# Kernel optimization log

Measured on AMD Instinct MI355X. Metric: run time of the kernel, lower is better.

Reference implementation:

```python
import jax, jax.numpy as jnp
import numpy as np

DT = 0.05      # bsde.delta_t
EPS = 1e-6     # BatchNormalization epsilon


def _bn(x, gamma, beta):
    # training-mode batch norm: statistics over the batch axis
    m = jnp.mean(x, axis=0, keepdims=True)
    v = jnp.var(x, axis=0, keepdims=True)
    return (x - m) * jax.lax.rsqrt(v + EPS) * gamma + beta


def _subnet(x, g0, b0, W0, g1, b1, W1, g2, b2, W2, bias2, g3, b3):
    # bn -> (dense -> bn -> relu) x 2 -> dense(+bias) -> bn
    x = _bn(x, g0, b0)
    x = jax.nn.relu(_bn(x @ W0, g1, b1))
    x = jax.nn.relu(_bn(x @ W1, g2, b2))
    x = _bn(x @ W2 + bias2, g3, b3)
    return x


def setup_inputs() -> dict:
    key = jax.random.key(0)
    B, D, N, H = 8192, 100, 20, 110
    T = N - 1  # number of subnets
    ks = jax.random.split(key, 18)
    u = lambda k, s, lo, hi: jax.random.uniform(k, s, jnp.float32, lo, hi)
    s_dh = np.sqrt(2.0 / (D + H)).astype(np.float32)
    s_hh = np.sqrt(2.0 / (H + H)).astype(np.float32)
    s_hd = np.sqrt(2.0 / (H + D)).astype(np.float32)
    return {
        "dw": jax.random.normal(ks[0], (B, D, N), jnp.float32) * np.sqrt(DT).astype(np.float32),
        "x": jax.random.normal(ks[1], (B, D, N + 1), jnp.float32),
        "mean_y_input": jax.random.normal(ks[2], (N,), jnp.float32),
        "y_init": u(ks[3], (1,), 0.0, 1.0),
        "z_init": u(ks[4], (1, D), -0.1, 0.1),
        "gamma0": u(ks[5], (T, D), 0.1, 0.5),
        "beta0": 0.1 * jax.random.normal(ks[6], (T, D), jnp.float32),
        "W0": s_dh * jax.random.normal(ks[7], (T, D, H), jnp.float32),
        "gamma1": u(ks[8], (T, H), 0.1, 0.5),
        "beta1": 0.1 * jax.random.normal(ks[9], (T, H), jnp.float32),
        "W1": s_hh * jax.random.normal(ks[10], (T, H, H), jnp.float32),
        "gamma2": u(ks[11], (T, H), 0.1, 0.5),
        "beta2": 0.1 * jax.random.normal(ks[12], (T, H), jnp.float32),
        "W2": s_hd * jax.random.normal(ks[13], (T, H, D), jnp.float32),
        "bias2": jnp.zeros((T, D), jnp.float32),
        "gamma3": u(ks[14], (T, D), 0.1, 0.5),
        "beta3": 0.1 * jax.random.normal(ks[15], (T, D), jnp.float32),
    }


def reference(dw, x, mean_y_input, y_init, z_init, gamma0, beta0, W0,
              gamma1, beta1, W1, gamma2, beta2, W2, bias2, gamma3, beta3):
    B, D, N = dw.shape
    T = N - 1
    # z at step t+1 depends only on x[:, :, t+1] and subnet t -> compute all in parallel
    x_steps = jnp.moveaxis(x[:, :, 1:N], 2, 0)  # [T, B, D]
    z_all = jax.vmap(_subnet)(x_steps, gamma0, beta0, W0, gamma1, beta1, W1,
                              gamma2, beta2, W2, bias2, gamma3, beta3) / D  # [T, B, D]
    z0 = jnp.broadcast_to(z_init, (B, D))          # all_one_vec @ z_init
    zs = jnp.concatenate([z0[None], z_all], axis=0)  # [N, B, D] (z used at each update)
    dw_steps = jnp.moveaxis(dw, 2, 0)               # [N, B, D]
    y0 = jnp.ones((B, 1), dw.dtype) * y_init

    def step(y, zd):
        z, dwt = zd
        # f_tf(t, x, y, z) = sin(y) for the SineBM equation
        y_new = y - DT * jnp.sin(y) + jnp.sum(z * dwt, axis=1, keepdims=True)
        return y_new, jnp.mean(y_new)

    y_final, means = jax.lax.scan(step, y0, (zs, dw_steps))
    mean_y = jnp.concatenate([jnp.mean(y0)[None], means[:T]])  # length N
    return y_final, mean_y
```

## Files before the change

### kernel.cpp

```cpp
#include <hip/hip_runtime.h>

typedef unsigned short u16;
typedef unsigned int   u32;

#define BATCH  8192
#define DIM    100
#define HID    110
#define TSUB   19
#define NSTEP  20
#define KP     128
#define NPAD   112
#define BN_EPS 1e-6f
#define DT_C   0.05f

#define SAB  1024
#define SAR  (BATCH / SAB)
#define SLICES 32

#define A3P  101

typedef __bf16 v8bf __attribute__((ext_vector_type(8)));
typedef float  v4f  __attribute__((ext_vector_type(4)));
typedef u16    u16x4 __attribute__((ext_vector_type(4)));

__device__ __forceinline__ u16 f2bf(float f) {
    u32 u = __float_as_uint(f);
    return (u16)((u + 0x7fffu + ((u >> 16) & 1u)) >> 16);
}
__device__ __forceinline__ float bf2f(u16 h) {
    return __uint_as_float(((u32)h) << 16);
}
__device__ __forceinline__ void acc4(float4& s, float4& q, float4 v) {
    s.x += v.x; s.y += v.y; s.z += v.z; s.w += v.w;
    q.x += v.x * v.x; q.y += v.y * v.y; q.z += v.z * v.z; q.w += v.w * v.w;
}

__global__ void statsA(const float* __restrict__ x, float* __restrict__ part,
                       u32* __restrict__ xT32) {
    __shared__ u16 xls[SAR][2112];
    const int tid = threadIdx.x;
    const int b0 = blockIdx.x * SAR;
    float4 s0 = {0,0,0,0}, q0 = {0,0,0,0};
    float4 s1 = {0,0,0,0}, q1 = {0,0,0,0};
    float4 s2 = {0,0,0,0}, q2 = {0,0,0,0};
#pragma unroll
    for (int r = 0; r < SAR; r++) {
        const float4* row = (const float4*)(x + (size_t)(b0 + r) * 2100);
        float4 v0 = row[tid];
        float4 v1 = row[tid + 256];
        acc4(s0, q0, v0);
        acc4(s1, q1, v1);
        u16x4 p0 = { f2bf(v0.x), f2bf(v0.y), f2bf(v0.z), f2bf(v0.w) };
        u16x4 p1 = { f2bf(v1.x), f2bf(v1.y), f2bf(v1.z), f2bf(v1.w) };
        *(u16x4*)&xls[r][tid * 4]        = p0;
        *(u16x4*)&xls[r][1024 + tid * 4] = p1;
        if (tid < 13) {
            float4 v2 = row[tid + 512];
            acc4(s2, q2, v2);
            u16x4 p2 = { f2bf(v2.x), f2bf(v2.y), f2bf(v2.z), f2bf(v2.w) };
            *(u16x4*)&xls[r][2048 + tid * 4] = p2;
        }
    }
    float* ps = part + (size_t)blockIdx.x * 4200;
    *(float4*)&ps[tid * 4]               = s0;
    *(float4*)&ps[1024 + tid * 4]        = s1;
    *(float4*)&ps[2100 + tid * 4]        = q0;
    *(float4*)&ps[2100 + 1024 + tid * 4] = q1;
    if (tid < 13) {
        *(float4*)&ps[2048 + tid * 4]        = s2;
        *(float4*)&ps[2100 + 2048 + tid * 4] = q2;
    }
    __syncthreads();
    const int TOT = TSUB * SAR * (NPAD / 2);
    for (int i = tid; i < TOT; i += 256) {
        int w = i % (NPAD / 2);
        int seg = i / (NPAD / 2);
        int r = seg % SAR, t = seg / SAR;
        int d0 = w * 2;
        u32 v = 0;
        if (d0 < DIM) {
            u16 lo = xls[r][d0 * 21 + t + 1];
            u16 hi = (d0 + 1 < DIM) ? xls[r][(d0 + 1) * 21 + t + 1] : (u16)0;
            v = (u32)lo | ((u32)hi << 16);
        }
        xT32[((size_t)t * BATCH + b0 + r) * (NPAD / 2) + w] = v;
    }
}

__global__ void statsB(const float* __restrict__ part, float* __restrict__ out) {
    int gid = blockIdx.x * 256 + threadIdx.x;
    if (gid >= 4200 * SLICES) return;
    int slice = gid / 4200;
    int o = gid - slice * 4200;
    const float* p = part + (size_t)slice * (SAB / SLICES) * 4200 + o;
    float acc = 0.f;
#pragma unroll 4
    for (int i = 0; i < SAB / SLICES; i++) acc += p[(size_t)i * 4200];
    atomicAdd(&out[o], acc);
}

__global__ void wtrans(const float* __restrict__ W0, const float* __restrict__ W1,
                       const float* __restrict__ W2, u16* __restrict__ WTsw) {
    __shared__ float lw[HID * HID];
    const int t = blockIdx.x, l = blockIdx.y, tid = threadIdx.x;
    const float* W; int K, N;
    if (l == 0)      { W = W0; K = DIM; N = HID; }
    else if (l == 1) { W = W1; K = HID; N = HID; }
    else             { W = W2; K = HID; N = DIM; }
    const float* Wt = W + (size_t)t * K * N;
    for (int i = tid; i < K * N; i += 256) lw[i] = Wt[i];
    __syncthreads();
    u16* out = WTsw + ((size_t)l * TSUB + t) * (NPAD * KP);
    for (int i = tid; i < NPAD * 16; i += 256) {
        int n = i / 16, p = i % 16;
        int kc = p ^ (n & 7);
        u16 o8[8];
#pragma unroll
        for (int j = 0; j < 8; j++) {
            int k = kc * 8 + j;
            float v = (k < K && n < N) ? lw[k * N + n] : 0.f;
            o8[j] = f2bf(v);
        }
        *(uint4*)&out[(size_t)n * KP + p * 8] = *(uint4*)o8;
    }
}

template <int KREAL, int NOUT, int IDXMODE, int RELU>
__global__ void gemm_kernel(const u16* __restrict__ Ain,
                            const u16* __restrict__ WTswL,
                            const float* __restrict__ sumIn,
                            const float* __restrict__ sqIn,
                            const float* __restrict__ gIn,
                            const float* __restrict__ bIn,
                            u16* __restrict__ Hout,
                            float* __restrict__ sumArr,
                            float* __restrict__ sqArr) {
    __shared__ __align__(16) u16 Alds[128 * KP];
    __shared__ __align__(16) u16 Blds[NPAD * KP];
    __shared__ float s_sum[NPAD], s_sq[NPAD];
    __shared__ float aAffL[KP], cAffL[KP];

    const int tid = threadIdx.x;
    const int mt = blockIdx.x;
    const int t  = blockIdx.y;
    const int brow0 = mt * 128;

    if (tid < NPAD) { s_sum[tid] = 0.f; s_sq[tid] = 0.f; }
    if (tid < KREAL) {
        int idx = (IDXMODE == 0) ? (tid * 21 + (t + 1)) : (t * KREAL + tid);
        float m = sumIn[idx] * (1.f / BATCH);
        float v = sqIn[idx] * (1.f / BATCH) - m * m;
        float rstd = rsqrtf(v + BN_EPS);
        float ga = gIn[t * KREAL + tid] * rstd;
        aAffL[tid] = ga;
        cAffL[tid] = bIn[t * KREAL + tid] - m * ga;
    }

    {
        const uint4* wsrc = (const uint4*)(WTswL + (size_t)t * NPAD * KP);
        uint4* bl = (uint4*)Blds;
#pragma unroll
        for (int i = 0; i < 7; i++) bl[tid + i * 256] = wsrc[tid + i * 256];
    }
    const int NCH = (KREAL + 7) / 8;
    for (int i = tid; i < 128 * (16 - NCH); i += 256) {
        int row = i / (16 - NCH);
        int kc  = NCH + i % (16 - NCH);
        uint4 z = {0, 0, 0, 0};
        *(uint4*)&Alds[row * KP + (kc ^ (row & 7)) * 8] = z;
    }
    __syncthreads();

    for (int cidx = tid; cidx < 128 * NCH; cidx += 256) {
        int row = cidx / NCH;
        int kc  = cidx % NCH;
        int k0  = kc * 8;
        const u16* hrow = Ain + ((size_t)t * BATCH + brow0 + row) * NPAD + k0;
        u16 hv[8];
        *(uint4*)hv = *(const uint4*)hrow;
        u16 pk[8];
#pragma unroll
        for (int j = 0; j < 8; j++) {
            int k = k0 + j;
            float av = (k < KREAL) ? fmaf(bf2f(hv[j]), aAffL[k], cAffL[k]) : 0.f;
            if (RELU) av = fmaxf(av, 0.f);
            pk[j] = f2bf(av);
        }
        *(uint4*)&Alds[row * KP + ((kc ^ (row & 7)) * 8)] = *(uint4*)pk;
    }
    __syncthreads();

    const int lane = tid & 63;
    const int wv   = tid >> 6;
    const int r0   = lane & 15;
    const int q    = lane >> 4;
    const int moff = wv * 32;

    v4f acc[2][7];
#pragma unroll
    for (int i = 0; i < 2; i++)
#pragma unroll
        for (int j = 0; j < 7; j++) { v4f z = {0.f, 0.f, 0.f, 0.f}; acc[i][j] = z; }

#pragma unroll
    for (int ks = 0; ks < 4; ks++) {
        int cbase = ks * 4 + q;
        v8bf afr[2];
#pragma unroll
        for (int mf = 0; mf < 2; mf++) {
            int row = moff + mf * 16 + r0;
            afr[mf] = *(const v8bf*)&Alds[row * KP + ((cbase ^ (row & 7)) * 8)];
        }
#pragma unroll
        for (int nf = 0; nf < 7; nf++) {
            int nr = nf * 16 + r0;
            v8bf bfr = *(const v8bf*)&Blds[nr * KP + ((cbase ^ (nr & 7)) * 8)];
            acc[0][nf] = __builtin_amdgcn_mfma_f32_16x16x32_bf16(afr[0], bfr, acc[0][nf], 0, 0, 0);
            acc[1][nf] = __builtin_amdgcn_mfma_f32_16x16x32_bf16(afr[1], bfr, acc[1][nf], 0, 0, 0);
        }
    }

#pragma unroll
    for (int mf = 0; mf < 2; mf++) {
#pragma unroll
        for (int nf = 0; nf < 7; nf++) {
            int n = nf * 16 + r0;
#pragma unroll
            for (int rg = 0; rg < 4; rg++) {
                int grow = brow0 + moff + mf * 16 + q * 4 + rg;
                Hout[((size_t)t * BATCH + grow) * NPAD + n] = f2bf(acc[mf][nf][rg]);
            }
        }
    }
#pragma unroll
    for (int nf = 0; nf < 7; nf++) {
        float cs = 0.f, cq = 0.f;
#pragma unroll
        for (int mf = 0; mf < 2; mf++)
#pragma unroll
            for (int rg = 0; rg < 4; rg++) {
                float vv = acc[mf][nf][rg];
                cs += vv; cq += vv * vv;
            }
        cs += __shfl_xor(cs, 16); cs += __shfl_xor(cs, 32);
        cq += __shfl_xor(cq, 16); cq += __shfl_xor(cq, 32);
        if (q == 0) {
            atomicAdd(&s_sum[nf * 16 + r0], cs);
            atomicAdd(&s_sq[nf * 16 + r0], cq);
        }
    }
    __syncthreads();
    if (tid < NOUT) {
        atomicAdd(&sumArr[t * NOUT + tid], s_sum[tid]);
        atomicAdd(&sqArr[t * NOUT + tid], s_sq[tid]);
    }
}

__global__ void scan_kernel(const float* __restrict__ dw,
                            const u16* __restrict__ zbuf,
                            const float* __restrict__ sum3, const float* __restrict__ sq3,
                            const float* __restrict__ g3, const float* __restrict__ b3,
                            const float* __restrict__ z_init, const float* __restrict__ y_init,
                            float* __restrict__ yout, float* __restrict__ meanout) {
    __shared__ float a3l[TSUB * A3P], c3l[TSUB * A3P], zil[DIM];
    __shared__ float bsum[NSTEP];
    const int tid = threadIdx.x;
    for (int i = tid; i < TSUB * DIM; i += 256) {
        int t = i / DIM, d = i - t * DIM;
        float m = sum3[i] * (1.f / BATCH);
        float v = sq3[i] * (1.f / BATCH) - m * m;
        float rstd = rsqrtf(v + BN_EPS);
        float ga = g3[i] * rstd;
        a3l[t * A3P + d] = ga * (1.f / DIM);
        c3l[t * A3P + d] = (b3[i] - m * ga) * (1.f / DIM);
    }
    if (tid < DIM) zil[tid] = z_init[tid];
    if (tid < NSTEP) bsum[tid] = 0.f;
    __syncthreads();

    const int wv = tid >> 6, lane = tid & 63;
    const int s = lane / 20, n = lane - s * 20;
    const int b = blockIdx.x * 4 + wv;

    float dot = 0.f;
    if (s < 3) {
        const int d0 = s * 32;
        const float* dwb = dw + (size_t)b * (DIM * NSTEP) + n;
        if (n == 0) {
            const int dend = (s == 2) ? DIM : d0 + 32;
#pragma unroll 4
            for (int d = d0; d < dend; d++) dot += zil[d] * dwb[d * NSTEP];
        } else {
            const int t = n - 1;
            const u16* zr = zbuf + ((size_t)t * BATCH + b) * NPAD + d0;
            const float* al = a3l + t * A3P + d0;
            const float* cl = c3l + t * A3P + d0;
#pragma unroll
            for (int dc = 0; dc < 4; dc++) {
                u16 hv[8];
                *(uint4*)hv = *(const uint4*)(zr + dc * 8);
                float wv8[8];
#pragma unroll
                for (int j = 0; j < 8; j++) wv8[j] = dwb[(d0 + dc * 8 + j) * NSTEP];
#pragma unroll
                for (int j = 0; j < 8; j++) {
                    int dd = dc * 8 + j;
                    dot += fmaf(bf2f(hv[j]), al[dd], cl[dd]) * wv8[j];
                }
            }
            if (s == 2) {
#pragma unroll
                for (int j = 0; j < 4; j++) {
                    float zv = fmaf(bf2f(zr[32 + j]), al[32 + j], cl[32 + j]);
                    dot += zv * dwb[(96 + j) * NSTEP];
                }
            }
        }
    }

    const float yi = y_init[0];
    float y = yi, ysave = 0.f;
#pragma unroll
    for (int i = 0; i < NSTEP; i++) {
        float dv = __shfl(dot, i, 64) + __shfl(dot, 20 + i, 64) + __shfl(dot, 40 + i, 64);
        y = y - DT_C * __sinf(y) + dv;
        if (i == n - 1) ysave = y;
    }
    if (s == 0 && n == 0) yout[b] = y;
    if (s == 0 && n >= 1) atomicAdd(&bsum[n], ysave);
    __syncthreads();
    if (tid >= 1 && tid < NSTEP) atomicAdd(&meanout[tid], bsum[tid] * (1.f / BATCH));
    if (blockIdx.x == 0 && tid == 0) meanout[0] = yi;
}

extern "C" void kernel_launch(void* const* d_in, const int* in_sizes, int n_in,
                              void* d_out, int out_size, void* d_ws, size_t ws_size,
                              hipStream_t stream) {
    const float* dw     = (const float*)d_in[0];
    const float* x      = (const float*)d_in[1];
    const float* y_init = (const float*)d_in[3];
    const float* z_init = (const float*)d_in[4];
    const float* g0 = (const float*)d_in[5];
    const float* b0 = (const float*)d_in[6];
    const float* W0 = (const float*)d_in[7];
    const float* g1 = (const float*)d_in[8];
    const float* b1 = (const float*)d_in[9];
    const float* W1 = (const float*)d_in[10];
    const float* g2 = (const float*)d_in[11];
    const float* b2 = (const float*)d_in[12];
    const float* W2 = (const float*)d_in[13];
    const float* g3 = (const float*)d_in[15];
    const float* b3 = (const float*)d_in[16];

    char* ws = (char*)d_ws;
    size_t off = 0;
    auto alloc = [&](size_t bytes) -> void* {
        off = (off + 255) & ~(size_t)255;
        void* p = ws + off;
        off += bytes;
        return p;
    };

    const int nStats = 4200 + TSUB * HID * 2 * 2 + TSUB * DIM * 2;
    float* statsBlk = (float*)alloc((size_t)nStats * 4);
    float* sum0 = statsBlk;            float* sq0  = sum0 + 2100;
    float* sum1 = sum0 + 4200;         float* sq1  = sum1 + TSUB * HID;
    float* sum2 = sq1 + TSUB * HID;    float* sq2  = sum2 + TSUB * HID;
    float* sum3 = sq2 + TSUB * HID;    float* sq3  = sum3 + TSUB * DIM;

    u16* WTsw = (u16*)alloc((size_t)3 * TSUB * NPAD * KP * 2);

    const size_t hBytes = (size_t)TSUB * BATCH * NPAD * 2;
    u16* h0 = (u16*)alloc(hBytes);
    u16* h1 = (u16*)alloc(hBytes);
    u16* outbuf = h0;
    float* part = (float*)h0;
    u32*  xT32  = (u32*)h1;

    float* yout = (float*)d_out;
    float* meanout = yout + BATCH;

    hipMemsetAsync(statsBlk, 0, (size_t)nStats * 4, stream);
    hipMemsetAsync(meanout, 0, NSTEP * 4, stream);

    wtrans<<<dim3(TSUB, 3), 256, 0, stream>>>(W0, W1, W2, WTsw);
    statsA<<<SAB, 256, 0, stream>>>(x, part, xT32);
    statsB<<<(4200 * SLICES + 255) / 256, 256, 0, stream>>>(part, sum0);

    const u16* xT = (const u16*)xT32;
    u16* WT0 = WTsw;
    u16* WT1 = WTsw + (size_t)TSUB * NPAD * KP;
    u16* WT2 = WTsw + (size_t)2 * TSUB * NPAD * KP;

    gemm_kernel<DIM, HID, 0, 0><<<dim3(64, TSUB), 256, 0, stream>>>(xT, WT0, sum0, sq0, g0, b0, h0, sum1, sq1);
    gemm_kernel<HID, HID, 1, 1><<<dim3(64, TSUB), 256, 0, stream>>>(h0, WT1, sum1, sq1, g1, b1, h1, sum2, sq2);
    gemm_kernel<HID, DIM, 1, 1><<<dim3(64, TSUB), 256, 0, stream>>>(h1, WT2, sum2, sq2, g2, b2, outbuf, sum3, sq3);

    scan_kernel<<<2048, 256, 0, stream>>>(dw, outbuf, sum3, sq3, g3, b3, z_init, y_init, yout, meanout);
}
```

Measured before the change: 200.5 us.

## Coalesce dw loads in scan kernel and stage BN-applied z through LDS

The scan kernel now has each lane read contiguous float4 chunks of the batch row of dw, instead of strided per-step loads. The decoded z values (bf16 with the final batch-norm affine applied) are staged per wave in shared memory, and each lane reads back pairs along the feature axis. Partial dot products for all 20 steps are reduced with a butterfly shuffle across the wave, and launch bounds are added. This removes uncoalesced stride-20 global reads but costs more shared memory and more shuffles, which may limit occupancy.

```diff
diff --git a/kernel.cpp b/kernel.cpp
--- a/kernel.cpp
+++ b/kernel.cpp
@@ -18,6 +18,7 @@
 #define SLICES 32
 
 #define A3P  101
+#define ZWP  104
 
 typedef __bf16 v8bf __attribute__((ext_vector_type(8)));
 typedef float  v4f  __attribute__((ext_vector_type(4)));
@@ -256,13 +257,15 @@
     }
 }
 
-__global__ void scan_kernel(const float* __restrict__ dw,
-                            const u16* __restrict__ zbuf,
-                            const float* __restrict__ sum3, const float* __restrict__ sq3,
-                            const float* __restrict__ g3, const float* __restrict__ b3,
-                            const float* __restrict__ z_init, const float* __restrict__ y_init,
-                            float* __restrict__ yout, float* __restrict__ meanout) {
-    __shared__ float a3l[TSUB * A3P], c3l[TSUB * A3P], zil[DIM];
+__global__ __launch_bounds__(256, 3)
+void scan_kernel(const float* __restrict__ dw,
+                 const u16* __restrict__ zbuf,
+                 const float* __restrict__ sum3, const float* __restrict__ sq3,
+                 const float* __restrict__ g3, const float* __restrict__ b3,
+                 const float* __restrict__ z_init, const float* __restrict__ y_init,
+                 float* __restrict__ yout, float* __restrict__ meanout) {
+    __shared__ float a3l[TSUB * A3P], c3l[TSUB * A3P];
+    __shared__ __align__(16) float zwf[4][NSTEP][ZWP];
     __shared__ float bsum[NSTEP];
     const int tid = threadIdx.x;
     for (int i = tid; i < TSUB * DIM; i += 256) {
@@ -274,60 +277,75 @@
         a3l[t * A3P + d] = ga * (1.f / DIM);
         c3l[t * A3P + d] = (b3[i] - m * ga) * (1.f / DIM);
     }
-    if (tid < DIM) zil[tid] = z_init[tid];
     if (tid < NSTEP) bsum[tid] = 0.f;
     __syncthreads();
 
     const int wv = tid >> 6, lane = tid & 63;
-    const int s = lane / 20, n = lane - s * 20;
     const int b = blockIdx.x * 4 + wv;
 
-    float dot = 0.f;
-    if (s < 3) {
-        const int d0 = s * 32;
-        const float* dwb = dw + (size_t)b * (DIM * NSTEP) + n;
-        if (n == 0) {
-            const int dend = (s == 2) ? DIM : d0 + 32;
-#pragma unroll 4
-            for (int d = d0; d < dend; d++) dot += zil[d] * dwb[d * NSTEP];
-        } else {
-            const int t = n - 1;
-            const u16* zr = zbuf + ((size_t)t * BATCH + b) * NPAD + d0;
-            const float* al = a3l + t * A3P + d0;
-            const float* cl = c3l + t * A3P + d0;
-#pragma unroll
-            for (int dc = 0; dc < 4; dc++) {
-                u16 hv[8];
-                *(uint4*)hv = *(const uint4*)(zr + dc * 8);
-                float wv8[8];
-#pragma unroll
-                for (int j = 0; j < 8; j++) wv8[j] = dwb[(d0 + dc * 8 + j) * NSTEP];
-#pragma unroll
-                for (int j = 0; j < 8; j++) {
-                    int dd = dc * 8 + j;
-                    dot += fmaf(bf2f(hv[j]), al[dd], cl[dd]) * wv8[j];
-                }
-            }
-            if (s == 2) {
-#pragma unroll
-                for (int j = 0; j < 4; j++) {
-                    float zv = fmaf(bf2f(zr[32 + j]), al[32 + j], cl[32 + j]);
-                    dot += zv * dwb[(96 + j) * NSTEP];
-                }
-            }
-        }
+    float4 w[10];
+    const float4* dwb4 = (const float4*)(dw + (size_t)b * (DIM * NSTEP));
+    if (lane < 50) {
+#pragma unroll
+        for (int j = 0; j < 10; j++) w[j] = dwb4[lane * 10 + j];
+    }
+
+    float (*zw)[ZWP] = zwf[wv];
+    for (int d = lane; d < ZWP; d += 64) zw[0][d] = (d < DIM) ? z_init[d] : 0.f;
+    for (int ci = lane; ci < TSUB * 13; ci += 64) {
+        int t = ci / 13, ch = ci - t * 13;
+        const u16* src = zbuf + ((size_t)t * BATCH + b) * NPAD + ch * 8;
+        u16 hv[8];
+        *(uint4*)hv = *(const uint4*)src;
+        float o[8];
+#pragma unroll
+        for (int k = 0; k < 8; k++) {
+            int d = ch * 8 + k;
+            int ds = (d < DIM) ? d : 0;
+            float av = fmaf(bf2f(hv[k]), a3l[t * A3P + ds], c3l[t * A3P + ds]);
+            o[k] = (d < DIM) ? av : 0.f;
+        }
+        *(float4*)&zw[t + 1][ch * 8]     = *(float4*)&o[0];
+        *(float4*)&zw[t + 1][ch * 8 + 4] = *(float4*)&o[4];
+    }
+    asm volatile("s_waitcnt lgkmcnt(0)" ::: "memory");
+
+    float2 zr[NSTEP];
+    if (lane < 50) {
+#pragma unroll
+        for (int n = 0; n < NSTEP; n++) zr[n] = *(const float2*)&zw[n][lane * 2];
+    }
+
+    float acc[NSTEP];
+#pragma unroll
+    for (int k = 0; k < NSTEP; k++) acc[k] = 0.f;
+    if (lane < 50) {
+#pragma unroll
+        for (int j = 0; j < 10; j++) {
+            const int sub = j / 5;
+            const int cb  = 4 * (j % 5);
+            acc[cb + 0] += w[j].x * (sub ? zr[cb + 0].y : zr[cb + 0].x);
+            acc[cb + 1] += w[j].y * (sub ? zr[cb + 1].y : zr[cb + 1].x);
+            acc[cb + 2] += w[j].z * (sub ? zr[cb + 2].y : zr[cb + 2].x);
+            acc[cb + 3] += w[j].w * (sub ? zr[cb + 3].y : zr[cb + 3].x);
+        }
+    }
+
+#pragma unroll
+    for (int m = 1; m < 64; m <<= 1) {
+#pragma unroll
+        for (int k = 0; k < NSTEP; k++) acc[k] += __shfl_xor(acc[k], m, 64);
     }
 
     const float yi = y_init[0];
     float y = yi, ysave = 0.f;
 #pragma unroll
     for (int i = 0; i < NSTEP; i++) {
-        float dv = __shfl(dot, i, 64) + __shfl(dot, 20 + i, 64) + __shfl(dot, 40 + i, 64);
-        y = y - DT_C * __sinf(y) + dv;
-        if (i == n - 1) ysave = y;
-    }
-    if (s == 0 && n == 0) yout[b] = y;
-    if (s == 0 && n >= 1) atomicAdd(&bsum[n], ysave);
+        y = y - DT_C * __sinf(y) + acc[i];
+        if (i == lane - 1) ysave = y;
+    }
+    if (lane == 0) yout[b] = y;
+    if (lane >= 1 && lane < NSTEP) atomicAdd(&bsum[lane], ysave);
     __syncthreads();
     if (tid >= 1 && tid < NSTEP) atomicAdd(&meanout[tid], bsum[tid] * (1.f / BATCH));
     if (blockIdx.x == 0 && tid == 0) meanout[0] = yi;
```

Result: no change. 202.2 us (+0.8%).
